# Performance work log

Hardware: AMD Instinct MI355X
Metric: run time of the kernel (lower is better)

Reference implementation:

```python
import jax, jax.numpy as jnp
import numpy as np

B, D, CIN, H, W = 2, 6, 3, 96, 96
DIM, NUM_HEADS, DEPTH = 144, 6, 2
WS = (2, 8, 8)   # window size (d, h, w)
SS = (1, 4, 4)   # shift size for odd blocks
HID = int(DIM * 2.0)
TBL = (2 * WS[0] - 1) * (2 * WS[1] - 1) * (2 * WS[2] - 1)  # 675
EPS = 1e-5


def _rpi(ws):
    # pairwise relative position index, same math as WindowAttention.get_position_index
    coords = np.stack(np.meshgrid(np.arange(ws[0]), np.arange(ws[1]), np.arange(ws[2]), indexing='ij'))
    cf = coords.reshape(3, -1).astype(np.int64)
    rc = (cf[:, :, None] - cf[:, None, :]).transpose(1, 2, 0)
    rc[..., 0] += ws[0] - 1
    rc[..., 1] += ws[1] - 1
    rc[..., 2] += ws[2] - 1
    rc[..., 0] *= (2 * ws[1] - 1) * (2 * ws[2] - 1)
    rc[..., 1] *= 2 * ws[2] - 1
    return rc.sum(-1)  # (N, N)


def _win_part_np(x, ws):
    b, d, h, w, c = x.shape
    x = x.reshape(b, d // ws[0], ws[0], h // ws[1], ws[1], w // ws[2], ws[2], c)
    return x.transpose(0, 1, 3, 5, 2, 4, 6, 7).reshape(-1, ws[0] * ws[1] * ws[2], c)


def _attn_mask(Dp, Hp, Wp, ws, ss):
    # static shift-window attention mask, same as compute_mask
    img = np.zeros((1, Dp, Hp, Wp, 1), np.float32)
    cnt = 0
    for d in (slice(-ws[0]), slice(-ws[0], -ss[0]), slice(-ss[0], None)):
        for h in (slice(-ws[1]), slice(-ws[1], -ss[1]), slice(-ss[1], None)):
            for w in (slice(-ws[2]), slice(-ws[2], -ss[2]), slice(-ss[2], None)):
                img[:, d, h, w, :] = cnt
                cnt += 1
    mw = _win_part_np(img, ws)[..., 0]  # (nW, N)
    am = mw[:, None, :] - mw[:, :, None]
    return np.where(am != 0, np.float32(-100.0), np.float32(0.0))


RPI = jnp.asarray(_rpi(WS))            # (N, N) int
MASK = jnp.asarray(_attn_mask(D, H, W, WS, SS))  # (nW, N, N)


def _ln(x, g, b):
    mu = jnp.mean(x, -1, keepdims=True)
    var = jnp.mean(jnp.square(x - mu), -1, keepdims=True)
    return (x - mu) * jax.lax.rsqrt(var + EPS) * g + b


def _win_part(x, ws):
    b, d, h, w, c = x.shape
    x = x.reshape(b, d // ws[0], ws[0], h // ws[1], ws[1], w // ws[2], ws[2], c)
    return x.transpose(0, 1, 3, 5, 2, 4, 6, 7).reshape(-1, ws[0] * ws[1] * ws[2], c)


def _win_rev(xw, ws, b, d, h, w):
    x = xw.reshape(b, d // ws[0], h // ws[1], w // ws[2], ws[0], ws[1], ws[2], -1)
    return x.transpose(0, 1, 4, 2, 5, 3, 6, 7).reshape(b, d, h, w, -1)


def _stl(x, i, shifted, params):
    # one Swin Transformer Layer; x: (B, D, H, W, C)
    n1g, n1b, qkvw, qkvb, rpb, projw, projb, n2g, n2b, fc1w, fc1b, fc2w, fc2b = params
    b, d, h, w, c = x.shape
    hd = c // NUM_HEADS
    scale = hd ** -0.5
    y = _ln(x, n1g[i], n1b[i])
    if shifted:
        y = jnp.roll(y, (-SS[0], -SS[1], -SS[2]), axis=(1, 2, 3))
    xw = _win_part(y, WS)  # (B_, N, C)
    B_, N, _ = xw.shape
    qkv = jnp.einsum('bnc,oc->bno', xw, qkvw[i]) + qkvb[i]
    qkv = qkv.reshape(B_, N, 3, NUM_HEADS, hd).transpose(2, 0, 3, 1, 4)
    q, k, v = qkv[0], qkv[1], qkv[2]
    attn = jnp.einsum('bhnd,bhmd->bhnm', q * scale, k)
    bias = rpb[i][RPI].transpose(2, 0, 1)  # (heads, N, N)
    attn = attn + bias[None]
    if shifted:
        nW = MASK.shape[0]
        attn = attn.reshape(B_ // nW, nW, NUM_HEADS, N, N) + MASK[None, :, None]
        attn = attn.reshape(B_, NUM_HEADS, N, N)
    attn = jax.nn.softmax(attn, axis=-1)
    out = jnp.einsum('bhnm,bhmd->bhnd', attn, v).transpose(0, 2, 1, 3).reshape(B_, N, c)
    out = jnp.einsum('bnc,oc->bno', out, projw[i]) + projb[i]
    y = _win_rev(out, WS, b, d, h, w)
    if shifted:
        y = jnp.roll(y, (SS[0], SS[1], SS[2]), axis=(1, 2, 3))
    x = x + y
    z = _ln(x, n2g[i], n2b[i])
    z = jnp.einsum('bdhwc,oc->bdhwo', z, fc1w[i]) + fc1b[i]
    z = jax.nn.gelu(z, approximate=False)
    z = jnp.einsum('bdhwo,co->bdhwc', z, fc2w[i]) + fc2b[i]
    return x + z


def setup_inputs() -> dict:
    key = jax.random.key(0)
    ks = jax.random.split(key, 8)
    s = 0.02
    return {
        'x': jax.random.normal(ks[0], (B, D, CIN, H, W), jnp.float32),
        'conv_w': jax.random.normal(ks[1], (DIM, CIN, 1, 3, 3), jnp.float32) * s,
        'conv_b': jnp.zeros((DIM,), jnp.float32),
        'ln0_g': jnp.ones((DIM,), jnp.float32),
        'ln0_b': jnp.zeros((DIM,), jnp.float32),
        'n1g': jnp.ones((DEPTH, DIM), jnp.float32),
        'n1b': jnp.zeros((DEPTH, DIM), jnp.float32),
        'qkvw': jax.random.normal(ks[2], (DEPTH, 3 * DIM, DIM), jnp.float32) * s,
        'qkvb': jnp.zeros((DEPTH, 3 * DIM), jnp.float32),
        'rpb': jax.random.normal(ks[3], (DEPTH, TBL, NUM_HEADS), jnp.float32) * s,
        'projw': jax.random.normal(ks[4], (DEPTH, DIM, DIM), jnp.float32) * s,
        'projb': jnp.zeros((DEPTH, DIM), jnp.float32),
        'n2g': jnp.ones((DEPTH, DIM), jnp.float32),
        'n2b': jnp.zeros((DEPTH, DIM), jnp.float32),
        'fc1w': jax.random.normal(ks[5], (DEPTH, HID, DIM), jnp.float32) * s,
        'fc1b': jnp.zeros((DEPTH, HID), jnp.float32),
        'fc2w': jax.random.normal(ks[6], (DEPTH, DIM, HID), jnp.float32) * s,
        'fc2b': jnp.zeros((DEPTH, DIM), jnp.float32),
        'lin_w': jax.random.normal(ks[7], (DIM, DIM), jnp.float32) * s,
        'lin_b': jnp.zeros((DIM,), jnp.float32),
        'ln1_g': jnp.ones((DIM,), jnp.float32),
        'ln1_b': jnp.zeros((DIM,), jnp.float32),
    }


def reference(x, conv_w, conv_b, ln0_g, ln0_b, n1g, n1b, qkvw, qkvb, rpb, projw, projb,
              n2g, n2b, fc1w, fc1b, fc2w, fc2b, lin_w, lin_b, ln1_g, ln1_b):
    # x: (n, d, c, h, w)
    y = x.transpose(0, 2, 1, 3, 4)  # n c d h w
    y = jax.lax.conv_general_dilated(
        y, conv_w, (1, 1, 1), [(0, 0), (1, 1), (1, 1)],
        dimension_numbers=('NCDHW', 'OIDHW', 'NCDHW')) + conv_b[None, :, None, None, None]
    y = y.transpose(0, 2, 3, 4, 1)  # n d h w c
    y = _ln(y, ln0_g, ln0_b)
    y = y.transpose(0, 4, 1, 2, 3)  # n c d h w
    params = (n1g, n1b, qkvw, qkvb, rpb, projw, projb, n2g, n2b, fc1w, fc1b, fc2w, fc2b)
    # RSTB (num_blocks = 1): residual group (STG of DEPTH STLs) + linear + skip
    f = y.transpose(0, 2, 3, 4, 1)  # b d h w c
    for i in range(DEPTH):
        f = _stl(f, i, i % 2 == 1, params)
    f = jnp.einsum('bdhwc,oc->bdhwo', f, lin_w) + lin_b
    y = y + f.transpose(0, 4, 1, 2, 3)
    # trailing LayerNorm and rearrange back to (n, d, c, h, w)
    out = _ln(y.transpose(0, 2, 3, 4, 1), ln1_g, ln1_b)
    return out.transpose(0, 1, 4, 2, 3)
```

## Files before the change

### kernel.cpp

```cpp
#include <hip/hip_runtime.h>
#include <math.h>

#define NTOK 110592
#define NWIN 864
#define TS   15925248

typedef unsigned short u16;
typedef unsigned int   u32;
typedef __attribute__((ext_vector_type(8))) short short8;
typedef __attribute__((ext_vector_type(4))) float float4v;

__device__ __forceinline__ float bf2f(u16 v) { return __uint_as_float(((u32)v) << 16); }
__device__ __forceinline__ u16 f2bf(float f) {
    u32 u = __float_as_uint(f);
    u32 r = u + 0x7fffu + ((u >> 16) & 1u);
    return (u16)(r >> 16);
}
__device__ __forceinline__ void unpack2(u32 u, float& lo, float& hi) {
    lo = __uint_as_float(u << 16);
    hi = __uint_as_float(u & 0xffff0000u);
}
__device__ __forceinline__ u32 pack2(float lo, float hi) {
    return (u32)f2bf(lo) | ((u32)f2bf(hi) << 16);
}
__device__ __forceinline__ float wave_sum(float v) {
    #pragma unroll
    for (int o = 32; o > 0; o >>= 1) v += __shfl_xor(v, o, 64);
    return v;
}

__device__ __forceinline__ void win_to_src(int tw, int shifted, int& sb, int& sd, int& sh, int& sw) {
    int n = tw & 127;
    int win = tw >> 7;
    int ww = win % 12;
    int wh = (win / 12) % 12;
    int rest = win / 144;
    int wd = rest % 3;
    sb = rest / 3;
    int ld = n >> 6, lh = (n >> 3) & 7, lw = n & 7;
    int dr = wd * 2 + ld, hr = wh * 8 + lh, wr = ww * 8 + lw;
    if (shifted) {
        sd = (dr + 1) % 6;
        sh = (hr + 4) % 96;
        sw = (wr + 4) % 96;
    } else {
        sd = dr; sh = hr; sw = wr;
    }
}

__device__ __forceinline__ int tok_region(int t, int wdn, int whn, int wwn) {
    int dr = wdn * 2 + (t >> 6), hr = whn * 8 + ((t >> 3) & 7), wr = wwn * 8 + (t & 7);
    int rd = (dr < 4) ? 0 : ((dr < 5) ? 1 : 2);
    int rh = (hr < 88) ? 0 : ((hr < 92) ? 1 : 2);
    int rw = (wr < 88) ? 0 : ((wr < 92) ? 1 : 2);
    return rd * 9 + rh * 3 + rw;
}

__global__ __launch_bounds__(256) void convert_weights(
    const float* __restrict__ qkvw, const float* __restrict__ projw,
    const float* __restrict__ fc1w, const float* __restrict__ fc2w,
    const float* __restrict__ linw, u16* __restrict__ wbuf,
    const float* __restrict__ rpb, float* __restrict__ bexp)
{
    int i = blockIdx.x * 256 + threadIdx.x;
    if (i < 124416) wbuf[i] = f2bf(qkvw[i]);
    else if (i < 165888) wbuf[i] = f2bf(projw[i - 124416]);
    else if (i < 248832) wbuf[i] = f2bf(fc1w[i - 165888]);
    else if (i < 331776) wbuf[i] = f2bf(fc2w[i - 248832]);
    else if (i < 352512) wbuf[i] = f2bf(linw[i - 331776]);
    else if (i < 549120) {
        int k = i - 352512;
        int n = k & 127, m = (k >> 7) & 127;
        int lh = k >> 14;
        int h = lh % 6, l = lh / 6;
        int rdi = (m >> 6) - (n >> 6) + 1;
        int rhi = ((m >> 3) & 7) - ((n >> 3) & 7) + 7;
        int rwi = (m & 7) - (n & 7) + 7;
        int bi = (rdi * 15 + rhi) * 15 + rwi;
        bexp[k] = rpb[l * 4050 + bi * 6 + h];
    }
}

__global__ __launch_bounds__(256) void conv_ln0_row(
    const float* __restrict__ x, const float* __restrict__ cw, const float* __restrict__ cb,
    const float* __restrict__ g0, const float* __restrict__ b0,
    float* __restrict__ y0)
{
    int bh = blockIdx.x;
    int h = bh % 96, bd = bh / 96;
    int b = bd / 6, d = bd - b * 6;
    __shared__ float ws[192][29];
    __shared__ float xsr[9][100];
    __shared__ float cbias[192], gg[144], bbv[144];
    int tid = threadIdx.x;

    for (int i = tid; i < 9 * 98; i += 256) {
        int row = i / 98, wx = i - row * 98;
        int ci = row / 3, kh = row - 3 * ci;
        int hh = h + kh - 1, wsrc = wx - 1;
        float v = 0.f;
        if (hh >= 0 && hh < 96 && wsrc >= 0 && wsrc < 96)
            v = x[((((size_t)b * 6 + d) * 3 + ci) * 96 + hh) * 96 + wsrc];
        xsr[row][wx] = v;
    }
    for (int i = tid; i < 192 * 27; i += 256) {
        int c = i / 27, j = i - c * 27;
        ws[c][j] = (c < 144) ? cw[c * 27 + j] : 0.f;
    }
    for (int i = tid; i < 192; i += 256) cbias[i] = (i < 144) ? cb[i] : 0.f;
    for (int i = tid; i < 144; i += 256) { gg[i] = g0[i]; bbv[i] = b0[i]; }
    __syncthreads();

    int wv = tid >> 6, lane = tid & 63;
    int p0 = wv * 24;

    float a0[24], a1[24], a2[24];
    #pragma unroll
    for (int k = 0; k < 24; k++) {
        a0[k] = cbias[lane]; a1[k] = cbias[lane + 64]; a2[k] = cbias[lane + 128];
    }

    for (int cikh = 0; cikh < 9; cikh++) {
        const float* xr = &xsr[cikh][p0];
        float xv[26];
        #pragma unroll
        for (int t = 0; t < 26; t++) xv[t] = xr[t];
        #pragma unroll
        for (int kw = 0; kw < 3; kw++) {
            int j = cikh * 3 + kw;
            float w0 = ws[lane][j], w1 = ws[lane + 64][j], w2 = ws[lane + 128][j];
            #pragma unroll
            for (int k = 0; k < 24; k++) {
                float xvv = xv[k + kw];
                a0[k] += w0 * xvv; a1[k] += w1 * xvv; a2[k] += w2 * xvv;
            }
        }
    }

    #pragma unroll
    for (int k = 0; k < 24; k++) {
        int p = p0 + k;
        float v0 = a0[k], v1 = a1[k];
        float v2m = (lane < 16) ? a2[k] : 0.f;
        float s  = wave_sum(v0 + v1 + v2m);
        float s2 = wave_sum(v0 * v0 + v1 * v1 + v2m * v2m);
        float mu = s * (1.f / 144.f);
        float rstd = rsqrtf(fmaxf(s2 * (1.f / 144.f) - mu * mu, 0.f) + 1e-5f);
        size_t o = ((size_t)bh * 96 + p) * 144;
        float r0 = (v0 - mu) * rstd * gg[lane] + bbv[lane];
        float r1 = (v1 - mu) * rstd * gg[lane + 64] + bbv[lane + 64];
        y0[o + lane] = r0;
        y0[o + lane + 64] = r1;
        if (lane < 16) {
            float r2 = (a2[k] - mu) * rstd * gg[lane + 128] + bbv[lane + 128];
            y0[o + lane + 128] = r2;
        }
    }
}

template<int MODE>
__global__ __launch_bounds__(256) void ln_gather(
    const float* __restrict__ in, u16* __restrict__ out,
    const float* __restrict__ g, const float* __restrict__ bt)
{
    int tok = blockIdx.x * 4 + (threadIdx.x >> 6);
    int lane = threadIdx.x & 63;
    int src;
    if (MODE == 0) src = tok;
    else {
        int b, d, h, w;
        win_to_src(tok, MODE == 2, b, d, h, w);
        src = ((b * 6 + d) * 96 + h) * 96 + w;
    }
    const float2* row = (const float2*)(in + (size_t)src * 144);
    float2 a = row[lane];
    float2 b2 = (lane < 8) ? row[64 + lane] : make_float2(0.f, 0.f);
    float s  = wave_sum(a.x + a.y + b2.x + b2.y);
    float s2 = wave_sum(a.x * a.x + a.y * a.y + b2.x * b2.x + b2.y * b2.y);
    float mu = s * (1.f / 144.f);
    float rstd = rsqrtf(fmaxf(s2 * (1.f / 144.f) - mu * mu, 0.f) + 1e-5f);
    const float2* g2 = (const float2*)g;
    const float2* t2 = (const float2*)bt;
    u32* orow = (u32*)(out + (size_t)tok * 144);
    float2 gg = g2[lane], tt = t2[lane];
    orow[lane] = pack2((a.x - mu) * rstd * gg.x + tt.x, (a.y - mu) * rstd * gg.y + tt.y);
    if (lane < 8) {
        float2 gh = g2[64 + lane], th = t2[64 + lane];
        orow[64 + lane] = pack2((b2.x - mu) * rstd * gh.x + th.x, (b2.y - mu) * rstd * gh.y + th.y);
    }
}

template<int AMODE, int EPI, int SHIFTED, int ADDBIAS, int KTILES, int NB>
__global__ __launch_bounds__(192) void mgemm(
    const void* __restrict__ Asrc, const u16* __restrict__ Wt, const float* __restrict__ bias,
    u16* __restrict__ outb, float* __restrict__ fres, const float* __restrict__ y0,
    int a_add, int a_ld, int w_ld, int o_ld, int o_add)
{
    __shared__ u16 As[64 * 152];
    int m0 = blockIdx.y * 64;
    int tid = threadIdx.x;
    int wv3 = tid / 64, lane = tid & 63;
    int mrow = lane & 15, quad = lane >> 4;
    const short8 z8 = {0, 0, 0, 0, 0, 0, 0, 0};

    float4v acc[4][3];

    auto zero_acc = [&]() {
        #pragma unroll
        for (int i = 0; i < 4; i++)
            #pragma unroll
            for (int j = 0; j < 3; j++) acc[i][j] = (float4v){0.f, 0.f, 0.f, 0.f};
    };

    auto stageA = [&](int kt) {
        if (AMODE == 2) {
            const u16* A = (const u16*)Asrc;
            for (int idx = tid; idx < 1152; idx += 192) {
                int r = idx / 18, c4 = idx - r * 18;
                *(short8*)&As[r * 152 + c4 * 8] =
                    *(const short8*)&A[(size_t)(a_add + m0 + r) * a_ld + kt * 144 + c4 * 8];
            }
        } else {
            const float* A = (const float*)Asrc;
            for (int idx = tid; idx < 2304; idx += 192) {
                int r = idx / 36, c4 = idx - r * 36;
                const float4* src4 = (const float4*)&A[(size_t)(a_add + m0 + r) * a_ld + kt * 144];
                float4 v = src4[c4];
                *(u32*)&As[r * 152 + c4 * 4]     = pack2(v.x, v.y);
                *(u32*)&As[r * 152 + c4 * 4 + 2] = pack2(v.z, v.w);
            }
        }
    };

    auto mfma_tile = [&](int n0, int kt) {
        const u16* Wg = Wt + (size_t)(n0 + wv3 * 48 + mrow) * w_ld + kt * 144;
        #pragma unroll
        for (int ks = 0; ks < 4; ks++) {
            int k0 = ks * 32;
            short8 af[4], bf[3];
            #pragma unroll
            for (int i = 0; i < 4; i++)
                af[i] = *(const short8*)&As[(i * 16 + mrow) * 152 + k0 + quad * 8];
            #pragma unroll
            for (int j = 0; j < 3; j++)
                bf[j] = *(const short8*)&Wg[(size_t)j * 16 * w_ld + k0 + quad * 8];
            #pragma unroll
            for (int i = 0; i < 4; i++)
                #pragma unroll
                for (int j = 0; j < 3; j++)
                    acc[i][j] = __builtin_amdgcn_mfma_f32_16x16x32_bf16(af[i], bf[j], acc[i][j], 0, 0, 0);
        }
        {
            bool tl = (quad < 2);
            short8 af[4], bf[3];
            #pragma unroll
            for (int i = 0; i < 4; i++)
                af[i] = tl ? *(const short8*)&As[(i * 16 + mrow) * 152 + 128 + quad * 8] : z8;
            #pragma unroll
            for (int j = 0; j < 3; j++)
                bf[j] = tl ? *(const short8*)&Wg[(size_t)j * 16 * w_ld + 128 + quad * 8] : z8;
            #pragma unroll
            for (int i = 0; i < 4; i++)
                #pragma unroll
                for (int j = 0; j < 3; j++)
                    acc[i][j] = __builtin_amdgcn_mfma_f32_16x16x32_bf16(af[i], bf[j], acc[i][j], 0, 0, 0);
        }
    };

    auto epilogue = [&](int n0) {
        #pragma unroll
        for (int i = 0; i < 4; i++) {
            #pragma unroll
            for (int reg = 0; reg < 4; reg++) {
                int m = m0 + i * 16 + quad * 4 + reg;
                int orow;
                if (EPI == 2 || EPI == 5) {
                    int b, d, h, w;
                    win_to_src(m, SHIFTED, b, d, h, w);
                    orow = ((b * 6 + d) * 96 + h) * 96 + w;
                } else orow = m + o_add;
                #pragma unroll
                for (int j = 0; j < 3; j++) {
                    int n = n0 + wv3 * 48 + j * 16 + mrow;
                    float v = acc[i][j][reg];
                    if (ADDBIAS) v += bias[n];
                    if (EPI == 1) v = 0.5f * v * (1.f + erff(v * 0.70710678118f));
                    if (EPI == 2 || EPI == 3) {
                        fres[(size_t)orow * 144 + n] += v;
                    } else if (EPI == 5) {
                        fres[(size_t)orow * 144 + n] = y0[(size_t)orow * 144 + n] + v;
                    } else if (EPI == 6) {
                        int slot = n / 144;
                        int hn = n - slot * 144;
                        int head = hn / 24, dd = hn - head * 24;
                        if (slot == 0) v *= 0.20412414523193154f;
                        outb[((size_t)head * o_ld + orow) * 72 + slot * 24 + dd] = f2bf(v);
                    } else {
                        if (EPI == 4) v += y0[(size_t)orow * o_ld + n];
                        outb[(size_t)orow * o_ld + n] = f2bf(v);
                    }
                }
            }
        }
    };

    if (NB == 1) {
        zero_acc();
        #pragma unroll
        for (int kt = 0; kt < KTILES; kt++) {
            if (kt) __syncthreads();
            stageA(kt);
            __syncthreads();
            mfma_tile(0, kt);
        }
        epilogue(0);
    } else {
        stageA(0);
        __syncthreads();
        #pragma unroll
        for (int nb = 0; nb < NB; nb++) {
            zero_acc();
            mfma_tile(nb * 144, 0);
            epilogue(nb * 144);
        }
    }
}

template<int SHIFTED>
__global__ __launch_bounds__(256) void attn_mfma(
    const u16* __restrict__ qkv,
    const float* __restrict__ bexp,
    u16* __restrict__ tok_out, int win_base, int chtok)
{
    int win = blockIdx.x;
    int head = blockIdx.y;
    __shared__ __align__(16) u16 Pb[4][2048];
    __shared__ __align__(16) u16 Vt[3072];
    __shared__ float invden_s[128];
    __shared__ u32 reg_pack[32];

    int tid = threadIdx.x;
    int wv = tid >> 6, lane = tid & 63;
    int c = lane & 15, quad = lane >> 4;
    int qbase = wv * 32;
    const short8 z8 = {0, 0, 0, 0, 0, 0, 0, 0};
    const float* bh_ = bexp + head * 16384;
    const u16* base = qkv + ((size_t)head * chtok + (size_t)win * 128) * 72;
    int cs = (c & 7) << 3;

    int wdn = 0, whn = 0, wwn = 0;
    if (SHIFTED) {
        int wib = (win_base + win) % 432;
        wwn = wib % 12; whn = (wib / 12) % 12; wdn = wib / 144;
    }

    if (tid < 128) {
        const u32* vsrc = (const u32*)(base + (size_t)tid * 72 + 48);
        #pragma unroll
        for (int i = 0; i < 12; i++) {
            u32 u = vsrc[i];
            int d0 = 2 * i, d1 = 2 * i + 1;
            Vt[((d0 << 7) + tid) ^ ((d0 & 7) << 3)] = (u16)(u & 0xffffu);
            Vt[((d1 << 7) + tid) ^ ((d1 & 7) << 3)] = (u16)(u >> 16);
        }
    }
    if (SHIFTED && tid < 32) {
        int t0 = tid * 4;
        reg_pack[tid] = (u32)tok_region(t0, wdn, whn, wwn)
                      | ((u32)tok_region(t0 + 1, wdn, whn, wwn) << 8)
                      | ((u32)tok_region(t0 + 2, wdn, whn, wwn) << 16)
                      | ((u32)tok_region(t0 + 3, wdn, whn, wwn) << 24);
    }
    __syncthreads();

    short8 aq[2];
    #pragma unroll
    for (int i = 0; i < 2; i++) {
        aq[i] = z8;
        if (quad < 3)
            aq[i] = *(const short8*)(base + (size_t)(qbase + i * 16 + c) * 72 + quad * 8);
    }

    float4v s_acc[2][8];
    #pragma unroll
    for (int i = 0; i < 2; i++)
        #pragma unroll
        for (int j = 0; j < 8; j++) s_acc[i][j] = (float4v){0.f, 0.f, 0.f, 0.f};

    #pragma unroll
    for (int j = 0; j < 8; j++) {
        short8 kf = z8;
        if (quad < 3)
            kf = *(const short8*)(base + (size_t)(j * 16 + c) * 72 + 24 + quad * 8);
        s_acc[0][j] = __builtin_amdgcn_mfma_f32_16x16x32_bf16(kf, aq[0], s_acc[0][j], 0, 0, 0);
        s_acc[1][j] = __builtin_amdgcn_mfma_f32_16x16x32_bf16(kf, aq[1], s_acc[1][j], 0, 0, 0);
    }

    float4v o_acc[2][2];
    #pragma unroll
    for (int i = 0; i < 2; i++)
        #pragma unroll
        for (int jv = 0; jv < 2; jv++) o_acc[i][jv] = (float4v){0.f, 0.f, 0.f, 0.f};

    #pragma unroll
    for (int i = 0; i < 2; i++) {
        int m = qbase + i * 16 + c;
        const float* brow = bh_ + m * 128;
        u32 myreg = SHIFTED ? (u32)tok_region(m, wdn, whn, wwn) : 0u;
        float den = 0.f;
        #pragma unroll
        for (int j = 0; j < 8; j++) {
            float4 bv = *(const float4*)(brow + j * 16 + quad * 4);
            float s0 = s_acc[i][j][0] + bv.x;
            float s1 = s_acc[i][j][1] + bv.y;
            float s2 = s_acc[i][j][2] + bv.z;
            float s3 = s_acc[i][j][3] + bv.w;
            if (SHIFTED) {
                u32 rv = reg_pack[j * 4 + quad];
                s0 += ((rv & 255u) == myreg) ? 0.f : -100.f;
                s1 += (((rv >> 8) & 255u) == myreg) ? 0.f : -100.f;
                s2 += (((rv >> 16) & 255u) == myreg) ? 0.f : -100.f;
                s3 += ((rv >> 24) == myreg) ? 0.f : -100.f;
            }
            float p0 = __expf(s0), p1 = __expf(s1), p2 = __expf(s2), p3 = __expf(s3);
            den += (p0 + p1) + (p2 + p3);
            u32 w0, w1;
            asm("v_cvt_pk_bf16_f32 %0, %1, %2" : "=v"(w0) : "v"(p0), "v"(p1));
            asm("v_cvt_pk_bf16_f32 %0, %1, %2" : "=v"(w1) : "v"(p2), "v"(p3));
            uint2 wpair = make_uint2(w0, w1);
            *(uint2*)&Pb[wv][((c << 7) + j * 16 + quad * 4) ^ cs] = wpair;
        }
        den += __shfl_xor(den, 16, 64);
        den += __shfl_xor(den, 32, 64);
        if (quad == 0) invden_s[m] = 1.f / den;

        #pragma unroll
        for (int ks = 0; ks < 4; ks++) {
            short8 pf  = *(const short8*)&Pb[wv][((c << 7) + ks * 32 + quad * 8) ^ cs];
            short8 vf0 = *(const short8*)&Vt[((c << 7) + ks * 32 + quad * 8) ^ cs];
            short8 vf1 = (c < 8) ? *(const short8*)&Vt[(((16 + c) << 7) + ks * 32 + quad * 8) ^ cs] : z8;
            o_acc[i][0] = __builtin_amdgcn_mfma_f32_16x16x32_bf16(pf, vf0, o_acc[i][0], 0, 0, 0);
            o_acc[i][1] = __builtin_amdgcn_mfma_f32_16x16x32_bf16(pf, vf1, o_acc[i][1], 0, 0, 0);
        }
    }

    float* ob = (float*)&Pb[wv][0];
    #pragma unroll
    for (int i = 0; i < 2; i++)
        #pragma unroll
        for (int jv = 0; jv < 2; jv++) {
            int d = jv * 16 + c;
            if (d < 24) {
                #pragma unroll
                for (int r = 0; r < 4; r++)
                    ob[(i * 16 + quad * 4 + r) * 26 + d] = o_acc[i][jv][r];
            }
        }
    __syncthreads();

    if (tid < 128) {
        const float2* ol = (const float2*)((const float*)&Pb[0][0]
                                           + (tid >> 5) * 1024 + (tid & 31) * 26);
        float inv = invden_s[tid];
        u32* orow = (u32*)tok_out + ((size_t)((win_base + win) * 128 + tid)) * 72 + head * 12;
        #pragma unroll
        for (int d2 = 0; d2 < 12; d2++) {
            float2 v = ol[d2];
            orow[d2] = pack2(v.x * inv, v.y * inv);
        }
    }
}

__global__ __launch_bounds__(256) void final_ln_out_kernel(
    const u16* __restrict__ gsrc, const float* __restrict__ g, const float* __restrict__ bt,
    float* __restrict__ out)
{
    int bh = blockIdx.x;
    int h = bh % 96, d = (bh / 96) % 6, b = bh / 576;
    __shared__ u16 tile[96][152];
    __shared__ float stat[96][2];
    const u16* src = gsrc + (size_t)bh * 96 * 144;
    for (int i = threadIdx.x; i < 1728; i += 256) {
        int wt = i / 18, c8 = i - wt * 18;
        *(short8*)&tile[wt][c8 * 8] = *(const short8*)&src[wt * 144 + c8 * 8];
    }
    __syncthreads();
    if (threadIdx.x < 96) {
        const u32* row = (const u32*)&tile[threadIdx.x][0];
        float s = 0.f, s2 = 0.f;
        #pragma unroll
        for (int j = 0; j < 72; j++) {
            float lo, hi; unpack2(row[j], lo, hi);
            s += lo + hi; s2 += lo * lo + hi * hi;
        }
        float mu = s * (1.f / 144.f);
        float var = s2 * (1.f / 144.f) - mu * mu;
        stat[threadIdx.x][0] = mu;
        stat[threadIdx.x][1] = rsqrtf(fmaxf(var, 0.f) + 1e-5f);
    }
    __syncthreads();
    size_t obase = ((size_t)(b * 6 + d) * 144) * 9216 + h * 96;
    for (int i = threadIdx.x; i < 96 * 144; i += blockDim.x) {
        int c = i / 96, wt = i - c * 96;
        out[obase + (size_t)c * 9216 + wt] =
            (bf2f(tile[wt][c]) - stat[wt][0]) * stat[wt][1] * g[c] + bt[c];
    }
}

extern "C" void kernel_launch(void* const* d_in, const int* in_sizes, int n_in,
                              void* d_out, int out_size, void* d_ws, size_t ws_size,
                              hipStream_t stream) {
    const float* x     = (const float*)d_in[0];
    const float* convw = (const float*)d_in[1];
    const float* convb = (const float*)d_in[2];
    const float* ln0g  = (const float*)d_in[3];
    const float* ln0b  = (const float*)d_in[4];
    const float* n1g   = (const float*)d_in[5];
    const float* n1b   = (const float*)d_in[6];
    const float* qkvw  = (const float*)d_in[7];
    const float* qkvb  = (const float*)d_in[8];
    const float* rpb   = (const float*)d_in[9];
    const float* projw = (const float*)d_in[10];
    const float* projb = (const float*)d_in[11];
    const float* n2g   = (const float*)d_in[12];
    const float* n2b   = (const float*)d_in[13];
    const float* fc1w  = (const float*)d_in[14];
    const float* fc1b  = (const float*)d_in[15];
    const float* fc2w  = (const float*)d_in[16];
    const float* fc2b  = (const float*)d_in[17];
    const float* linw  = (const float*)d_in[18];
    const float* linb  = (const float*)d_in[19];
    const float* ln1g  = (const float*)d_in[20];
    const float* ln1b  = (const float*)d_in[21];

    char* wp = (char*)d_ws;
    float* f    = (float*)wp;             wp += (size_t)TS * 4;
    u16*   tok  = (u16*)wp;               wp += (size_t)TS * 2;
    u16*   wbuf = (u16*)wp;               wp += 352512ull * 2;
    float* bexp = (float*)wp;             wp += 196608ull * 4;
    u16*   qkvbuf = (u16*)wp;
    size_t rest = ws_size - (size_t)(wp - (char*)d_ws);
    int nch = (rest >= (size_t)NTOK * 432 * 2) ? 1
            : (rest >= (size_t)NTOK * 216 * 2) ? 2 : 4;
    int nm  = (rest >= (size_t)NTOK * 288 * 2) ? 1
            : (rest >= (size_t)NTOK * 144 * 2) ? 2 : 3;
    float* y0 = (float*)d_out;

    convert_weights<<<2145, 256, 0, stream>>>(qkvw, projw, fc1w, fc2w, linw, wbuf, rpb, bexp);
    conv_ln0_row<<<1152, 256, 0, stream>>>(x, convw, convb, ln0g, ln0b, y0);

    for (int layer = 0; layer < 2; ++layer) {
        const u16* qw  = wbuf + (size_t)layer * 62208;
        const u16* pw  = wbuf + 124416 + (size_t)layer * 20736;
        const u16* f1w = wbuf + 165888 + (size_t)layer * 41472;
        const u16* f2w = wbuf + 248832 + (size_t)layer * 41472;
        const float* qb  = qkvb + (size_t)layer * 432;
        const float* pb  = projb + (size_t)layer * 144;
        const float* g1  = n1g + layer * 144;
        const float* b1  = n1b + layer * 144;
        const float* g2  = n2g + layer * 144;
        const float* b2  = n2b + layer * 144;
        const float* f1b = fc1b + (size_t)layer * 288;
        const float* f2b = fc2b + (size_t)layer * 144;
        const float* bx  = bexp + (size_t)layer * 98304;

        if (layer == 0) ln_gather<1><<<NTOK / 4, 256, 0, stream>>>(y0, tok, g1, b1);
        else            ln_gather<2><<<NTOK / 4, 256, 0, stream>>>(f, tok, g1, b1);

        int chtok = NTOK / nch, chwin = NWIN / nch;
        for (int c = 0; c < nch; c++) {
            mgemm<2, 6, 0, 1, 1, 3><<<dim3(1, chtok / 64), 192, 0, stream>>>(
                tok, qw, qb, qkvbuf, nullptr, nullptr,
                c * chtok, 144, 144, chtok, 0);
            if (layer == 0)
                attn_mfma<0><<<dim3(chwin, 6), 256, 0, stream>>>(qkvbuf, bx, tok, c * chwin, chtok);
            else
                attn_mfma<1><<<dim3(chwin, 6), 256, 0, stream>>>(qkvbuf, bx, tok, c * chwin, chtok);
        }

        if (layer == 0)
            mgemm<2, 5, 0, 1, 1, 1><<<dim3(1, NTOK / 64), 192, 0, stream>>>(
                tok, pw, pb, nullptr, f, y0, 0, 144, 144, 144, 0);
        else
            mgemm<2, 2, 1, 1, 1, 1><<<dim3(1, NTOK / 64), 192, 0, stream>>>(
                tok, pw, pb, nullptr, f, nullptr, 0, 144, 144, 144, 0);

        ln_gather<0><<<NTOK / 4, 256, 0, stream>>>(f, tok, g2, b2);

        int fcch = NTOK / nm;
        for (int c = 0; c < nm; c++) {
            int mst = c * fcch;
            mgemm<2, 1, 0, 1, 1, 2><<<dim3(1, fcch / 64), 192, 0, stream>>>(
                tok, f1w, f1b, qkvbuf, nullptr, nullptr, mst, 144, 144, 288, 0);
            mgemm<2, 3, 0, 1, 2, 1><<<dim3(1, fcch / 64), 192, 0, stream>>>(
                qkvbuf, f2w, f2b, nullptr, f, nullptr, 0, 288, 288, 144, mst);
        }
    }

    mgemm<0, 4, 0, 1, 1, 1><<<dim3(1, NTOK / 64), 192, 0, stream>>>(
        f, wbuf + 331776, linb, tok, nullptr, y0, 0, 144, 144, 144, 0);

    final_ln_out_kernel<<<2 * 6 * 96, 256, 0, stream>>>(tok, ln1g, ln1b, (float*)d_out);
}
```

Baseline: 852.6 us.

## Split GEMM N-blocks across grid and write attention output head-major

The GEMM kernel no longer loops over several 144-wide output blocks inside one workgroup. Those blocks now go into blockIdx.x, which triples or doubles the grid for the QKV and FC1 GEMMs but means each block restages its A tile. The attention kernel now writes its output in a per-chunk head-major layout with contiguous 24-wide rows. A new A-loading mode in the projection GEMM gathers that layout back into token rows. This changes the write pattern of attention and the read pattern of the projection GEMM together.

```diff
diff --git a/kernel.cpp b/kernel.cpp
--- a/kernel.cpp
+++ b/kernel.cpp
@@ -190,38 +190,52 @@
     }
 }
 
-template<int AMODE, int EPI, int SHIFTED, int ADDBIAS, int KTILES, int NB>
+template<int AMODE, int EPI, int SHIFTED, int ADDBIAS, int KTILES>
 __global__ __launch_bounds__(192) void mgemm(
     const void* __restrict__ Asrc, const u16* __restrict__ Wt, const float* __restrict__ bias,
     u16* __restrict__ outb, float* __restrict__ fres, const float* __restrict__ y0,
     int a_add, int a_ld, int w_ld, int o_ld, int o_add)
 {
     __shared__ u16 As[64 * 152];
-    int m0 = blockIdx.y * 64;
+    int m0 = blockIdx.y * 64, n0 = blockIdx.x * 144;
     int tid = threadIdx.x;
     int wv3 = tid / 64, lane = tid & 63;
     int mrow = lane & 15, quad = lane >> 4;
     const short8 z8 = {0, 0, 0, 0, 0, 0, 0, 0};
 
     float4v acc[4][3];
-
-    auto zero_acc = [&]() {
-        #pragma unroll
-        for (int i = 0; i < 4; i++)
-            #pragma unroll
-            for (int j = 0; j < 3; j++) acc[i][j] = (float4v){0.f, 0.f, 0.f, 0.f};
-    };
-
-    auto stageA = [&](int kt) {
+    #pragma unroll
+    for (int i = 0; i < 4; i++)
+        #pragma unroll
+        for (int j = 0; j < 3; j++) acc[i][j] = (float4v){0.f, 0.f, 0.f, 0.f};
+
+    #pragma unroll
+    for (int kt = 0; kt < KTILES; kt++) {
+        if (kt) __syncthreads();
         if (AMODE == 2) {
             const u16* A = (const u16*)Asrc;
+            #pragma unroll
             for (int idx = tid; idx < 1152; idx += 192) {
                 int r = idx / 18, c4 = idx - r * 18;
                 *(short8*)&As[r * 152 + c4 * 8] =
                     *(const short8*)&A[(size_t)(a_add + m0 + r) * a_ld + kt * 144 + c4 * 8];
             }
+        } else if (AMODE == 3) {
+            const u16* A = (const u16*)Asrc;
+            int chtok = a_ld;
+            int cc = m0 / chtok;
+            int t0 = m0 - cc * chtok;
+            const u16* Ac = A + (size_t)cc * chtok * 144;
+            #pragma unroll
+            for (int idx = tid; idx < 1152; idx += 192) {
+                int r = idx / 18, c4 = idx - r * 18;
+                int hh = c4 / 3, sub = c4 - hh * 3;
+                *(short8*)&As[r * 152 + c4 * 8] =
+                    *(const short8*)&Ac[((size_t)hh * chtok + t0 + r) * 24 + sub * 8];
+            }
         } else {
             const float* A = (const float*)Asrc;
+            #pragma unroll
             for (int idx = tid; idx < 2304; idx += 192) {
                 int r = idx / 36, c4 = idx - r * 36;
                 const float4* src4 = (const float4*)&A[(size_t)(a_add + m0 + r) * a_ld + kt * 144];
@@ -230,10 +244,10 @@
                 *(u32*)&As[r * 152 + c4 * 4 + 2] = pack2(v.z, v.w);
             }
         }
-    };
-
-    auto mfma_tile = [&](int n0, int kt) {
+        __syncthreads();
+
         const u16* Wg = Wt + (size_t)(n0 + wv3 * 48 + mrow) * w_ld + kt * 144;
+
         #pragma unroll
         for (int ks = 0; ks < 4; ks++) {
             int k0 = ks * 32;
@@ -265,63 +279,40 @@
                 for (int j = 0; j < 3; j++)
                     acc[i][j] = __builtin_amdgcn_mfma_f32_16x16x32_bf16(af[i], bf[j], acc[i][j], 0, 0, 0);
         }
-    };
-
-    auto epilogue = [&](int n0) {
-        #pragma unroll
-        for (int i = 0; i < 4; i++) {
-            #pragma unroll
-            for (int reg = 0; reg < 4; reg++) {
-                int m = m0 + i * 16 + quad * 4 + reg;
-                int orow;
-                if (EPI == 2 || EPI == 5) {
-                    int b, d, h, w;
-                    win_to_src(m, SHIFTED, b, d, h, w);
-                    orow = ((b * 6 + d) * 96 + h) * 96 + w;
-                } else orow = m + o_add;
-                #pragma unroll
-                for (int j = 0; j < 3; j++) {
-                    int n = n0 + wv3 * 48 + j * 16 + mrow;
-                    float v = acc[i][j][reg];
-                    if (ADDBIAS) v += bias[n];
-                    if (EPI == 1) v = 0.5f * v * (1.f + erff(v * 0.70710678118f));
-                    if (EPI == 2 || EPI == 3) {
-                        fres[(size_t)orow * 144 + n] += v;
-                    } else if (EPI == 5) {
-                        fres[(size_t)orow * 144 + n] = y0[(size_t)orow * 144 + n] + v;
-                    } else if (EPI == 6) {
-                        int slot = n / 144;
-                        int hn = n - slot * 144;
-                        int head = hn / 24, dd = hn - head * 24;
-                        if (slot == 0) v *= 0.20412414523193154f;
-                        outb[((size_t)head * o_ld + orow) * 72 + slot * 24 + dd] = f2bf(v);
-                    } else {
-                        if (EPI == 4) v += y0[(size_t)orow * o_ld + n];
-                        outb[(size_t)orow * o_ld + n] = f2bf(v);
-                    }
+    }
+
+    #pragma unroll
+    for (int i = 0; i < 4; i++) {
+        #pragma unroll
+        for (int reg = 0; reg < 4; reg++) {
+            int m = m0 + i * 16 + quad * 4 + reg;
+            int orow;
+            if (EPI == 2 || EPI == 5) {
+                int b, d, h, w;
+                win_to_src(m, SHIFTED, b, d, h, w);
+                orow = ((b * 6 + d) * 96 + h) * 96 + w;
+            } else orow = m + o_add;
+            #pragma unroll
+            for (int j = 0; j < 3; j++) {
+                int n = n0 + wv3 * 48 + j * 16 + mrow;
+                float v = acc[i][j][reg];
+                if (ADDBIAS) v += bias[n];
+                if (EPI == 1) v = 0.5f * v * (1.f + erff(v * 0.70710678118f));
+                if (EPI == 2 || EPI == 3) {
+                    fres[(size_t)orow * 144 + n] += v;
+                } else if (EPI == 5) {
+                    fres[(size_t)orow * 144 + n] = y0[(size_t)orow * 144 + n] + v;
+                } else if (EPI == 6) {
+                    int slot = n / 144;
+                    int hn = n - slot * 144;
+                    int head = hn / 24, dd = hn - head * 24;
+                    if (slot == 0) v *= 0.20412414523193154f;
+                    outb[((size_t)head * o_ld + orow) * 72 + slot * 24 + dd] = f2bf(v);
+                } else {
+                    if (EPI == 4) v += y0[(size_t)orow * o_ld + n];
+                    outb[(size_t)orow * o_ld + n] = f2bf(v);
                 }
             }
-        }
-    };
-
-    if (NB == 1) {
-        zero_acc();
-        #pragma unroll
-        for (int kt = 0; kt < KTILES; kt++) {
-            if (kt) __syncthreads();
-            stageA(kt);
-            __syncthreads();
-            mfma_tile(0, kt);
-        }
-        epilogue(0);
-    } else {
-        stageA(0);
-        __syncthreads();
-        #pragma unroll
-        for (int nb = 0; nb < NB; nb++) {
-            zero_acc();
-            mfma_tile(nb * 144, 0);
-            epilogue(nb * 144);
         }
     }
 }
@@ -330,7 +321,8 @@
 __global__ __launch_bounds__(256) void attn_mfma(
     const u16* __restrict__ qkv,
     const float* __restrict__ bexp,
-    u16* __restrict__ tok_out, int win_base, int chtok)
+    u16* __restrict__ tok_out,
+    int win_base, int chtok)
 {
     int win = blockIdx.x;
     int head = blockIdx.y;
@@ -462,7 +454,7 @@
         const float2* ol = (const float2*)((const float*)&Pb[0][0]
                                            + (tid >> 5) * 1024 + (tid & 31) * 26);
         float inv = invden_s[tid];
-        u32* orow = (u32*)tok_out + ((size_t)((win_base + win) * 128 + tid)) * 72 + head * 12;
+        u32* orow = (u32*)tok_out + ((size_t)head * chtok + (size_t)win * 128 + tid) * 12;
         #pragma unroll
         for (int d2 = 0; d2 < 12; d2++) {
             float2 v = ol[d2];
@@ -569,35 +561,36 @@
 
         int chtok = NTOK / nch, chwin = NWIN / nch;
         for (int c = 0; c < nch; c++) {
-            mgemm<2, 6, 0, 1, 1, 3><<<dim3(1, chtok / 64), 192, 0, stream>>>(
+            mgemm<2, 6, 0, 1, 1><<<dim3(3, chtok / 64), 192, 0, stream>>>(
                 tok, qw, qb, qkvbuf, nullptr, nullptr,
                 c * chtok, 144, 144, chtok, 0);
+            u16* ob = tok + (size_t)c * chtok * 144;
             if (layer == 0)
-                attn_mfma<0><<<dim3(chwin, 6), 256, 0, stream>>>(qkvbuf, bx, tok, c * chwin, chtok);
+                attn_mfma<0><<<dim3(chwin, 6), 256, 0, stream>>>(qkvbuf, bx, ob, c * chwin, chtok);
             else
-                attn_mfma<1><<<dim3(chwin, 6), 256, 0, stream>>>(qkvbuf, bx, tok, c * chwin, chtok);
+                attn_mfma<1><<<dim3(chwin, 6), 256, 0, stream>>>(qkvbuf, bx, ob, c * chwin, chtok);
         }
 
         if (layer == 0)
-            mgemm<2, 5, 0, 1, 1, 1><<<dim3(1, NTOK / 64), 192, 0, stream>>>(
-                tok, pw, pb, nullptr, f, y0, 0, 144, 144, 144, 0);
+            mgemm<3, 5, 0, 1, 1><<<dim3(1, NTOK / 64), 192, 0, stream>>>(
+                tok, pw, pb, nullptr, f, y0, 0, chtok, 144, 144, 0);
         else
-            mgemm<2, 2, 1, 1, 1, 1><<<dim3(1, NTOK / 64), 192, 0, stream>>>(
-                tok, pw, pb, nullptr, f, nullptr, 0, 144, 144, 144, 0);
+            mgemm<3, 2, 1, 1, 1><<<dim3(1, NTOK / 64), 192, 0, stream>>>(
+                tok, pw, pb, nullptr, f, nullptr, 0, chtok, 144, 144, 0);
 
         ln_gather<0><<<NTOK / 4, 256, 0, stream>>>(f, tok, g2, b2);
 
         int fcch = NTOK / nm;
         for (int c = 0; c < nm; c++) {
             int mst = c * fcch;
-            mgemm<2, 1, 0, 1, 1, 2><<<dim3(1, fcch / 64), 192, 0, stream>>>(
+            mgemm<2, 1, 0, 1, 1><<<dim3(2, fcch / 64), 192, 0, stream>>>(
                 tok, f1w, f1b, qkvbuf, nullptr, nullptr, mst, 144, 144, 288, 0);
-            mgemm<2, 3, 0, 1, 2, 1><<<dim3(1, fcch / 64), 192, 0, stream>>>(
+            mgemm<2, 3, 0, 1, 2><<<dim3(1, fcch / 64), 192, 0, stream>>>(
                 qkvbuf, f2w, f2b, nullptr, f, nullptr, 0, 288, 288, 144, mst);
         }
     }
 
-    mgemm<0, 4, 0, 1, 1, 1><<<dim3(1, NTOK / 64), 192, 0, stream>>>(
+    mgemm<0, 4, 0, 1, 1><<<dim3(1, NTOK / 64), 192, 0, stream>>>(
         f, wbuf + 331776, linb, tok, nullptr, y0, 0, 144, 144, 144, 0);
 
     final_ln_out_kernel<<<2 * 6 * 96, 256, 0, stream>>>(tok, ln1g, ln1b, (float*)d_out);
```

Result: no change. 839.9 us (-1.5%).
